# Kernel optimization log

Hardware: AMD Instinct MI355X
Metric: run time of the kernel (lower is better)

Reference implementation:

```python
import jax, jax.numpy as jnp
import numpy as np

B, T, C = 128, 256, 384
H, D = 6, 64

def setup_inputs() -> dict:
    key = jax.random.key(0)
    ks = jax.random.split(key, 6)
    s = 1.0 / np.sqrt(C)
    return {
        "x": jax.random.normal(ks[0], (B, T, C), dtype=jnp.float32),
        "Wq": jax.random.normal(ks[1], (H, C, D), dtype=jnp.float32) * s,
        "Wk": jax.random.normal(ks[2], (H, C, D), dtype=jnp.float32) * s,
        "Wv": jax.random.normal(ks[3], (H, C, D), dtype=jnp.float32) * s,
        "Wp": jax.random.normal(ks[4], (C, C), dtype=jnp.float32) * s,
        "bp": jnp.zeros((C,), dtype=jnp.float32),
    }

def reference(x, Wq, Wk, Wv, Wp, bp):
    # per-head projections (all heads at once): [B,T,C] x [H,C,D] -> [B,H,T,D]
    q = jnp.einsum("btc,hcd->bhtd", x, Wq)
    k = jnp.einsum("btc,hcd->bhtd", x, Wk)
    v = jnp.einsum("btc,hcd->bhtd", x, Wv)
    scale = 1.0 / jnp.sqrt(jnp.asarray(D, dtype=x.dtype))
    # scores [B,H,T,T], causal mask, softmax
    wei = jnp.einsum("bhqd,bhkd->bhqk", q, k) * scale
    causal = jnp.tril(jnp.ones((T, T), dtype=bool))
    wei = jnp.where(causal, wei, -jnp.inf)
    wei = jax.nn.softmax(wei, axis=-1)
    # dropout layers are identity in eval mode
    out = jnp.einsum("bhqk,bhkd->bhqd", wei, v)
    # concat heads: [B,T,H*D]
    out = out.transpose(0, 2, 1, 3).reshape(B, T, H * D)
    return out @ Wp + bp
```

## Files before the change

### kernel.cpp

```cpp
#include <hip/hip_runtime.h>
#include <stdint.h>


typedef __attribute__((ext_vector_type(8))) short bf16x8;
typedef __attribute__((ext_vector_type(4))) float f32x4;
typedef __attribute__((ext_vector_type(16))) float f32x16;

__device__ __forceinline__ unsigned short f2b(float f) {
    union { float f; unsigned int u; } v; v.f = f;
    unsigned int u = v.u + 0x7fffu + ((v.u >> 16) & 1u);
    return (unsigned short)(u >> 16);
}

__device__ __forceinline__ unsigned int pk2(float lo, float hi) {
    return (unsigned int)f2b(lo) | ((unsigned int)f2b(hi) << 16);
}

__device__ __forceinline__ void gload_lds16(const void* g, void* lds) {
    auto gp = reinterpret_cast<const __attribute__((address_space(1))) uint32_t*>(
        reinterpret_cast<uintptr_t>(g));
    auto lp = reinterpret_cast<__attribute__((address_space(3))) uint32_t*>(
        reinterpret_cast<uintptr_t>(lds));
    __builtin_amdgcn_global_load_lds(gp, lp, 16, 0, 0);
}

#define SBAR0() __builtin_amdgcn_sched_barrier(0)


__global__ void cvt_w_kernel(const float* __restrict__ Wq, const float* __restrict__ Wk,
                             const float* __restrict__ Wv, const float* __restrict__ Wp,
                             unsigned short* __restrict__ wt, unsigned short* __restrict__ wpt) {
    int i = blockIdx.x * 256 + threadIdx.x;
    if (i >= 589824) return;
    if (i < 442368) {
        int j = i / 384, c = i - j * 384;
        int p = j / 384, rem = j - p * 384;
        int h = rem >> 6, d = rem & 63;
        const float* W = (p == 0) ? Wq : ((p == 1) ? Wk : Wv);
        wt[i] = f2b(W[(size_t)(h * 384 + c) * 64 + d]);
    } else {
        int i2 = i - 442368;
        int n = i2 / 384, c = i2 - n * 384;
        wpt[i2] = f2b(Wp[(size_t)c * 384 + n]);
    }
}


__global__ __launch_bounds__(256, 4) void gemm_qkv(
    const float* __restrict__ x,
    const unsigned short* __restrict__ wt,
    unsigned short* __restrict__ qO,
    unsigned short* __restrict__ kO,
    unsigned short* __restrict__ vO)
{
    extern __shared__ __align__(16) unsigned short smem[];
    unsigned short* As0 = smem;
    unsigned short* As1 = smem + 4096;
    unsigned short* Bs0 = smem + 8192;
    unsigned short* Bs1 = smem + 12288;

    const int tid  = threadIdx.x;
    const int lane = tid & 63;
    const int w    = tid >> 6;
    const int wm = w >> 1, wn = w & 1;

    const int flat = blockIdx.y * 9 + blockIdx.x;
    const int swz = (flat & 7) * 288 + (flat >> 3);
    const int bx = swz % 9, by = swz / 9;
    const int col0 = bx * 128;
    const int row0 = by * 128;

    f32x4 acc[4][4];
#pragma unroll
    for (int mf = 0; mf < 4; ++mf)
#pragma unroll
        for (int nf = 0; nf < 4; ++nf)
#pragma unroll
            for (int r = 0; r < 4; ++r) acc[mf][nf][r] = 0.f;

    const int ci0 = tid;
    const int ci1 = tid + 256;
    const float* aS0 = x + (size_t)(row0 + (ci0 >> 2)) * 384 + (ci0 & 3) * 8;
    const float* aS1 = x + (size_t)(row0 + (ci1 >> 2)) * 384 + (ci1 & 3) * 8;
    const unsigned short* bS0 = wt + (size_t)(col0 + (ci0 >> 2)) * 384 + (ci0 & 3) * 8;
    const unsigned short* bS1 = wt + (size_t)(col0 + (ci1 >> 2)) * 384 + (ci1 & 3) * 8;
    const int cb = w * 64;

    float4 aReg0, aReg1, aReg2, aReg3;
    auto LOADA = [&](int kt) {
        const float* p0 = aS0 + kt * 32;
        const float* p1 = aS1 + kt * 32;
        aReg0 = *(const float4*)(p0);
        aReg1 = *(const float4*)(p0 + 4);
        aReg2 = *(const float4*)(p1);
        aReg3 = *(const float4*)(p1 + 4);
    };
    auto WRITEA = [&](unsigned short* As) {
        uint4 w0 = make_uint4(pk2(aReg0.x, aReg0.y), pk2(aReg0.z, aReg0.w),
                              pk2(aReg1.x, aReg1.y), pk2(aReg1.z, aReg1.w));
        uint4 w1 = make_uint4(pk2(aReg2.x, aReg2.y), pk2(aReg2.z, aReg2.w),
                              pk2(aReg3.x, aReg3.y), pk2(aReg3.z, aReg3.w));
        *(uint4*)&As[ci0 * 8] = w0;
        *(uint4*)&As[ci1 * 8] = w1;
    };
    auto STAGEB = [&](unsigned short* Bs, int kt) {
        gload_lds16(bS0 + kt * 32, Bs + (cb + 0) * 8);
        gload_lds16(bS1 + kt * 32, Bs + (cb + 256) * 8);
    };
    auto COMPUTE = [&](const unsigned short* A, const unsigned short* B) {
        bf16x8 aF[4], bF[4];
#pragma unroll
        for (int mf = 0; mf < 4; ++mf)
            aF[mf] = *(const bf16x8*)&A[(wm * 64 + mf * 16 + (lane & 15)) * 32 + (lane >> 4) * 8];
#pragma unroll
        for (int nf = 0; nf < 4; ++nf)
            bF[nf] = *(const bf16x8*)&B[(wn * 64 + nf * 16 + (lane & 15)) * 32 + (lane >> 4) * 8];
#pragma unroll
        for (int mf = 0; mf < 4; ++mf)
#pragma unroll
            for (int nf = 0; nf < 4; ++nf)
                acc[mf][nf] = __builtin_amdgcn_mfma_f32_16x16x32_bf16(aF[mf], bF[nf], acc[mf][nf], 0, 0, 0);
    };

    LOADA(0);
    STAGEB(Bs0, 0);
    WRITEA(As0);
    __syncthreads();

    for (int t = 0; t < 12; ++t) {
        unsigned short* Acur = (t & 1) ? As1 : As0;
        unsigned short* Bcur = (t & 1) ? Bs1 : Bs0;
        unsigned short* Anx  = (t & 1) ? As0 : As1;
        unsigned short* Bnx  = (t & 1) ? Bs0 : Bs1;
        if (t < 11) {
            LOADA(t + 1);
            STAGEB(Bnx, t + 1);
        }
        COMPUTE(Acur, Bcur);
        if (t < 11) WRITEA(Anx);
        __syncthreads();
    }

    unsigned short* Ct = smem;
    const int co = tid & 15;
    const int rr = tid >> 4;
    const int colg = col0 + co * 8;
    const int p = colg / 384;
    const int rem = colg - p * 384;
    const int h = rem >> 6;
    const int d = rem & 63;
    unsigned short* dst = (p == 0) ? qO : ((p == 1) ? kO : vO);

#pragma unroll
    for (int ph = 0; ph < 2; ++ph) {
        if (wm == ph) {
#pragma unroll
            for (int mf = 0; mf < 4; ++mf)
#pragma unroll
                for (int nf = 0; nf < 4; ++nf)
#pragma unroll
                    for (int r = 0; r < 4; ++r)
                        Ct[(mf * 16 + (lane >> 4) * 4 + r) * 136 + wn * 64 + nf * 16 + (lane & 15)] =
                            f2b(acc[mf][nf][r]);
        }
        __syncthreads();
#pragma unroll
        for (int it = 0; it < 4; ++it) {
            const int r_loc = it * 16 + rr;
            const int m = row0 + ph * 64 + r_loc;
            const int b = m >> 8, t = m & 255;
            uint4 val = *(const uint4*)&Ct[r_loc * 136 + co * 8];
            *(uint4*)&dst[(size_t)((b * 6 + h) * 256 + t) * 64 + d] = val;
        }
        __syncthreads();
    }
}


__global__ __launch_bounds__(512, 4) void attn_kernel(
    const unsigned short* __restrict__ Qg,
    const unsigned short* __restrict__ Kg,
    const unsigned short* __restrict__ Vg,
    unsigned short* __restrict__ Og)
{
    extern __shared__ __align__(16) unsigned short asmem[];
    unsigned short* Ks = asmem;
    unsigned short* Vs = asmem + 256 * 72;
    unsigned short* Ot = asmem;
    const int bh = blockIdx.x;
    const int b = bh / 6, h = bh - b * 6;
    const int tid = threadIdx.x;
    const int lane = tid & 63;
    const int w = tid >> 6;
    const int lo = lane & 31, hi = lane >> 5;

    const unsigned short* kg = Kg + (size_t)bh * 256 * 64;
#pragma unroll
    for (int j = 0; j < 4; ++j) {
        int chunk = tid + 512 * j;
        int key = chunk >> 3, dc = (chunk & 7) * 8;
        *(uint4*)&Ks[key * 72 + dc] = *(const uint4*)&kg[key * 64 + dc];
    }
    {
        const unsigned short* vg = Vg + (size_t)bh * 256 * 64;
        uint32_t* Vs32 = (uint32_t*)Vs;
#pragma unroll
        for (int i = 0; i < 2; ++i) {
            int u = tid + 512 * i;
            int t2 = (u & 31) | ((u >> 8) << 5);
            int dm = (u >> 5) & 7;
            uint4 r0 = *(const uint4*)&vg[(2 * t2 + 0) * 64 + dm * 8];
            uint4 r1 = *(const uint4*)&vg[(2 * t2 + 1) * 64 + dm * 8];
            const unsigned short* e0 = (const unsigned short*)&r0;
            const unsigned short* e1 = (const unsigned short*)&r1;
#pragma unroll
            for (int j = 0; j < 8; ++j)
                Vs32[(dm * 8 + j) * 132 + t2] = (uint32_t)e0[j] | ((uint32_t)e1[j] << 16);
        }
    }
    __syncthreads();

    const int q0 = w * 32;
    const unsigned short* qg = Qg + (size_t)bh * 256 * 64 + (size_t)(q0 + lo) * 64 + hi * 8;
    bf16x8 qF[4];
#pragma unroll
    for (int dc = 0; dc < 4; ++dc) qF[dc] = *(const bf16x8*)(qg + dc * 16);

    float m = -1e30f, ssum = 0.f;
    f32x16 o0, o1;
#pragma unroll
    for (int r = 0; r < 16; ++r) { o0[r] = 0.f; o1[r] = 0.f; }

    for (int kt = 0; kt <= w; ++kt) {
        f32x16 s;
#pragma unroll
        for (int r = 0; r < 16; ++r) s[r] = 0.f;
#pragma unroll
        for (int dc = 0; dc < 4; ++dc) {
            bf16x8 aK = *(const bf16x8*)&Ks[(kt * 32 + lo) * 72 + dc * 16 + hi * 8];
            s = __builtin_amdgcn_mfma_f32_32x32x16_bf16(aK, qF[dc], s, 0, 0, 0);
        }
        float p[16];
        float pmax = -1e30f;
        const bool diag = (kt == w);
#pragma unroll
        for (int r = 0; r < 16; ++r) {
            float sv = s[r] * 0.125f;
            const int keyl = (r & 3) + 8 * (r >> 2) + 4 * hi;
            if (diag && keyl > lo) sv = -1e30f;
            p[r] = sv;
            pmax = fmaxf(pmax, sv);
        }
        pmax = fmaxf(pmax, __shfl_xor(pmax, 32, 64));
        const float mn = fmaxf(m, pmax);
        const float sf = __expf(m - mn);
        m = mn;
        ssum *= sf;
#pragma unroll
        for (int r = 0; r < 16; ++r) { o0[r] *= sf; o1[r] *= sf; }
        float rs = 0.f;
#pragma unroll
        for (int r = 0; r < 16; ++r) { p[r] = __expf(p[r] - m); rs += p[r]; }
        rs += __shfl_xor(rs, 32, 64);
        ssum += rs;

        union { unsigned short u[16]; bf16x8 v[2]; } P;
        {
            float recv[4];
#pragma unroll
            for (int j2 = 0; j2 < 4; ++j2) {
                float sendv = hi ? p[j2] : p[4 + j2];
                recv[j2] = __shfl_xor(sendv, 32, 64);
            }
#pragma unroll
            for (int i = 0; i < 4; ++i) P.u[i]     = f2b(hi ? recv[i] : p[i]);
#pragma unroll
            for (int i = 0; i < 4; ++i) P.u[4 + i] = f2b(hi ? p[4 + i] : recv[i]);
        }
        {
            float recv[4];
#pragma unroll
            for (int j2 = 0; j2 < 4; ++j2) {
                float sendv = hi ? p[8 + j2] : p[12 + j2];
                recv[j2] = __shfl_xor(sendv, 32, 64);
            }
#pragma unroll
            for (int i = 0; i < 4; ++i) P.u[8 + i]  = f2b(hi ? recv[i] : p[8 + i]);
#pragma unroll
            for (int i = 0; i < 4; ++i) P.u[12 + i] = f2b(hi ? p[12 + i] : recv[i]);
        }

#pragma unroll
        for (int kc = 0; kc < 2; ++kc) {
            bf16x8 aV0 = *(const bf16x8*)&Vs[lo * 264 + kt * 32 + kc * 16 + hi * 8];
            o0 = __builtin_amdgcn_mfma_f32_32x32x16_bf16(aV0, P.v[kc], o0, 0, 0, 0);
            bf16x8 aV1 = *(const bf16x8*)&Vs[(32 + lo) * 264 + kt * 32 + kc * 16 + hi * 8];
            o1 = __builtin_amdgcn_mfma_f32_32x32x16_bf16(aV1, P.v[kc], o1, 0, 0, 0);
        }
    }

    __syncthreads();
    const float inv = 1.f / ssum;
    {
        uint32_t* ot32 = (uint32_t*)&Ot[w * 32 * 72];
#pragma unroll
        for (int g = 0; g < 4; ++g) {
            const int dbase0 = 8 * g + 4 * hi;
            uint32_t w0 = pk2(o0[4 * g + 0] * inv, o0[4 * g + 1] * inv);
            uint32_t w1 = pk2(o0[4 * g + 2] * inv, o0[4 * g + 3] * inv);
            int dw = lo * 36 + (dbase0 >> 1);
            ot32[dw] = w0;
            ot32[dw + 1] = w1;
            uint32_t w2 = pk2(o1[4 * g + 0] * inv, o1[4 * g + 1] * inv);
            uint32_t w3 = pk2(o1[4 * g + 2] * inv, o1[4 * g + 3] * inv);
            int dw1 = lo * 36 + ((32 + dbase0) >> 1);
            ot32[dw1] = w2;
            ot32[dw1 + 1] = w3;
        }
    }
    __syncthreads();
    {
        const unsigned short* ot = &Ot[w * 32 * 72];
        const int q = lane >> 1;
        const int half = (lane & 1) * 32;
        unsigned short* og = Og + (size_t)(b * 256 + q0 + q) * 384 + h * 64 + half;
#pragma unroll
        for (int jj = 0; jj < 4; ++jj) {
            uint4 val = *(const uint4*)&ot[q * 72 + half + jj * 8];
            *(uint4*)&og[jj * 8] = val;
        }
    }
}


__global__ __launch_bounds__(256, 3) void gemm_proj(
    const unsigned short* __restrict__ ob,
    const unsigned short* __restrict__ wpt,
    const float* __restrict__ bp,
    float* __restrict__ out)
{
    __shared__ __align__(16) unsigned short As[3][128 * 32];
    __shared__ __align__(16) unsigned short Bs[3][128 * 32];
    const int tid  = threadIdx.x;
    const int lane = tid & 63;
    const int w    = tid >> 6;
    const int wm = w >> 1, wn = w & 1;

    const int flat = blockIdx.y * 3 + blockIdx.x;
    const int swz = (flat & 7) * 96 + (flat >> 3);
    const int bx = swz % 3, by = swz / 3;
    const int col0 = bx * 128;
    const int row0 = by * 128;

    const unsigned short* Abase = ob  + (size_t)row0 * 384;
    const unsigned short* Bbase = wpt + (size_t)col0 * 384;

    f32x4 acc[4][4];
#pragma unroll
    for (int mf = 0; mf < 4; ++mf)
#pragma unroll
        for (int nf = 0; nf < 4; ++nf)
#pragma unroll
            for (int r = 0; r < 4; ++r) acc[mf][nf][r] = 0.f;

    const int ci0 = tid;
    const int ci1 = tid + 256;
    const unsigned short* aSrc0 = Abase + (size_t)(ci0 >> 2) * 384 + (ci0 & 3) * 8;
    const unsigned short* aSrc1 = Abase + (size_t)(ci1 >> 2) * 384 + (ci1 & 3) * 8;
    const unsigned short* bSrc0 = Bbase + (size_t)(ci0 >> 2) * 384 + (ci0 & 3) * 8;
    const unsigned short* bSrc1 = Bbase + (size_t)(ci1 >> 2) * 384 + (ci1 & 3) * 8;
    const int cb = w * 64;

    auto STAGE = [&](int buf, int kt) {
        const int k0_ = kt * 32;
        gload_lds16(aSrc0 + k0_, (unsigned short*)As[buf] + (cb + 0) * 8);
        gload_lds16(bSrc0 + k0_, (unsigned short*)Bs[buf] + (cb + 0) * 8);
        gload_lds16(aSrc1 + k0_, (unsigned short*)As[buf] + (cb + 256) * 8);
        gload_lds16(bSrc1 + k0_, (unsigned short*)Bs[buf] + (cb + 256) * 8);
    };

    auto COMPUTE = [&](int buf) {
        const unsigned short* A = As[buf];
        const unsigned short* B = Bs[buf];
        bf16x8 aF[4], bF[4];
#pragma unroll
        for (int mf = 0; mf < 4; ++mf)
            aF[mf] = *(const bf16x8*)&A[(wm * 64 + mf * 16 + (lane & 15)) * 32 + (lane >> 4) * 8];
#pragma unroll
        for (int nf = 0; nf < 4; ++nf)
            bF[nf] = *(const bf16x8*)&B[(wn * 64 + nf * 16 + (lane & 15)) * 32 + (lane >> 4) * 8];
#pragma unroll
        for (int mf = 0; mf < 4; ++mf)
#pragma unroll
            for (int nf = 0; nf < 4; ++nf)
                acc[mf][nf] = __builtin_amdgcn_mfma_f32_16x16x32_bf16(aF[mf], bF[nf], acc[mf][nf], 0, 0, 0);
    };

    STAGE(0, 0);
    STAGE(1, 1);
    SBAR0();
    int bufS = 2, bufC = 0;
    for (int t = 0; t < 10; ++t) {
        STAGE(bufS, t + 2);
        bufS = (bufS == 2) ? 0 : bufS + 1;
        SBAR0();
        asm volatile("s_waitcnt vmcnt(8)" ::: "memory");
        SBAR0();
        __builtin_amdgcn_s_barrier();
        SBAR0();
        COMPUTE(bufC);
        bufC = (bufC == 2) ? 0 : bufC + 1;
        SBAR0();
        __builtin_amdgcn_s_barrier();
        SBAR0();
    }
    asm volatile("s_waitcnt vmcnt(4)" ::: "memory");
    SBAR0();
    __builtin_amdgcn_s_barrier();
    SBAR0();
    COMPUTE(1);
    SBAR0();
    __builtin_amdgcn_s_barrier();
    SBAR0();
    asm volatile("s_waitcnt vmcnt(0)" ::: "memory");
    SBAR0();
    __builtin_amdgcn_s_barrier();
    SBAR0();
    COMPUTE(2);

#pragma unroll
    for (int nf = 0; nf < 4; ++nf) {
        const int col = col0 + wn * 64 + nf * 16 + (lane & 15);
        const float bias = bp[col];
#pragma unroll
        for (int mf = 0; mf < 4; ++mf) {
            const int mbase = row0 + wm * 64 + mf * 16 + ((lane >> 4) * 4);
#pragma unroll
            for (int r = 0; r < 4; ++r) {
                const int mrow = mbase + r;
                out[(size_t)mrow * 384 + col] = acc[mf][nf][r] + bias;
            }
        }
    }
}


extern "C" void kernel_launch(void* const* d_in, const int* in_sizes, int n_in,
                              void* d_out, int out_size, void* d_ws, size_t ws_size,
                              hipStream_t stream) {
    const float* x  = (const float*)d_in[0];
    const float* Wq = (const float*)d_in[1];
    const float* Wk = (const float*)d_in[2];
    const float* Wv = (const float*)d_in[3];
    const float* Wp = (const float*)d_in[4];
    const float* bp = (const float*)d_in[5];
    float* out = (float*)d_out;

    char* ws = (char*)d_ws;
    unsigned short* ob  = (unsigned short*)(ws);
    unsigned short* qb  = (unsigned short*)(ws + 25165824);
    unsigned short* kb  = (unsigned short*)(ws + 50331648);
    unsigned short* vb  = (unsigned short*)(ws + 75497472);
    unsigned short* wt  = (unsigned short*)(ws + 100663296);
    unsigned short* wpt = (unsigned short*)(ws + 101548032);

    cvt_w_kernel<<<2304, 256, 0, stream>>>(Wq, Wk, Wv, Wp, wt, wpt);
    gemm_qkv<<<dim3(9, 256), 256, 32768, stream>>>(x, wt, qb, kb, vb);
    attn_kernel<<<768, 512, 70656, stream>>>(qb, kb, vb, ob);
    gemm_proj<<<dim3(3, 256), 256, 0, stream>>>(ob, wpt, bp, out);
}
```

Baseline: 107.8 us.

## Use hardware bf16 pack, MFMA priority, lazy softmax rescale, swizzled LDS in projection

In the QKV GEMM, the manual round-to-nearest bf16 packing is replaced by the v_cvt_pk_bf16_f32 instruction. In the attention loop, MFMA blocks are wrapped in s_setprio, and the online-softmax rescale of the output accumulators now runs only when the running max grows by more than 8. The output projection GEMM XOR-swizzles its global-to-LDS chunk placement and fragment reads to reduce LDS bank conflicts. The lazy rescale keeps a stale max, so exp values can reach up to e^8 before normalisation. That is safe in fp32 but changes the bf16 rounding of P slightly.

Measured after the change: 105.2 us (median of 3 runs). -2.5%, faster.

```diff
diff --git a/kernel.cpp b/kernel.cpp
--- a/kernel.cpp
+++ b/kernel.cpp
@@ -14,6 +14,12 @@
 
 __device__ __forceinline__ unsigned int pk2(float lo, float hi) {
     return (unsigned int)f2b(lo) | ((unsigned int)f2b(hi) << 16);
+}
+
+__device__ __forceinline__ uint32_t cvtpk(float lo, float hi) {
+    uint32_t r;
+    asm("v_cvt_pk_bf16_f32 %0, %1, %2" : "=v"(r) : "v"(lo), "v"(hi));
+    return r;
 }
 
 __device__ __forceinline__ void gload_lds16(const void* g, void* lds) {
@@ -96,10 +102,11 @@
         aReg3 = *(const float4*)(p1 + 4);
     };
     auto WRITEA = [&](unsigned short* As) {
-        uint4 w0 = make_uint4(pk2(aReg0.x, aReg0.y), pk2(aReg0.z, aReg0.w),
-                              pk2(aReg1.x, aReg1.y), pk2(aReg1.z, aReg1.w));
-        uint4 w1 = make_uint4(pk2(aReg2.x, aReg2.y), pk2(aReg2.z, aReg2.w),
-                              pk2(aReg3.x, aReg3.y), pk2(aReg3.z, aReg3.w));
+        uint4 w0, w1;
+        w0.x = cvtpk(aReg0.x, aReg0.y); w0.y = cvtpk(aReg0.z, aReg0.w);
+        w0.z = cvtpk(aReg1.x, aReg1.y); w0.w = cvtpk(aReg1.z, aReg1.w);
+        w1.x = cvtpk(aReg2.x, aReg2.y); w1.y = cvtpk(aReg2.z, aReg2.w);
+        w1.z = cvtpk(aReg3.x, aReg3.y); w1.w = cvtpk(aReg3.z, aReg3.w);
         *(uint4*)&As[ci0 * 8] = w0;
         *(uint4*)&As[ci1 * 8] = w1;
     };
@@ -235,11 +242,13 @@
         f32x16 s;
 #pragma unroll
         for (int r = 0; r < 16; ++r) s[r] = 0.f;
+        __builtin_amdgcn_s_setprio(1);
 #pragma unroll
         for (int dc = 0; dc < 4; ++dc) {
             bf16x8 aK = *(const bf16x8*)&Ks[(kt * 32 + lo) * 72 + dc * 16 + hi * 8];
             s = __builtin_amdgcn_mfma_f32_32x32x16_bf16(aK, qF[dc], s, 0, 0, 0);
         }
+        __builtin_amdgcn_s_setprio(0);
         float p[16];
         float pmax = -1e30f;
         const bool diag = (kt == w);
@@ -252,12 +261,13 @@
             pmax = fmaxf(pmax, sv);
         }
         pmax = fmaxf(pmax, __shfl_xor(pmax, 32, 64));
-        const float mn = fmaxf(m, pmax);
-        const float sf = __expf(m - mn);
-        m = mn;
-        ssum *= sf;
-#pragma unroll
-        for (int r = 0; r < 16; ++r) { o0[r] *= sf; o1[r] *= sf; }
+        if (pmax > m + 8.f) {
+            const float sf = __expf(m - pmax);
+            m = pmax;
+            ssum *= sf;
+#pragma unroll
+            for (int r = 0; r < 16; ++r) { o0[r] *= sf; o1[r] *= sf; }
+        }
         float rs = 0.f;
 #pragma unroll
         for (int r = 0; r < 16; ++r) { p[r] = __expf(p[r] - m); rs += p[r]; }
@@ -290,6 +300,7 @@
             for (int i = 0; i < 4; ++i) P.u[12 + i] = f2b(hi ? p[12 + i] : recv[i]);
         }
 
+        __builtin_amdgcn_s_setprio(1);
 #pragma unroll
         for (int kc = 0; kc < 2; ++kc) {
             bf16x8 aV0 = *(const bf16x8*)&Vs[lo * 264 + kt * 32 + kc * 16 + hi * 8];
@@ -297,6 +308,7 @@
             bf16x8 aV1 = *(const bf16x8*)&Vs[(32 + lo) * 264 + kt * 32 + kc * 16 + hi * 8];
             o1 = __builtin_amdgcn_mfma_f32_32x32x16_bf16(aV1, P.v[kc], o1, 0, 0, 0);
         }
+        __builtin_amdgcn_s_setprio(0);
     }
 
     __syncthreads();
@@ -365,10 +377,12 @@
 
     const int ci0 = tid;
     const int ci1 = tid + 256;
-    const unsigned short* aSrc0 = Abase + (size_t)(ci0 >> 2) * 384 + (ci0 & 3) * 8;
-    const unsigned short* aSrc1 = Abase + (size_t)(ci1 >> 2) * 384 + (ci1 & 3) * 8;
-    const unsigned short* bSrc0 = Bbase + (size_t)(ci0 >> 2) * 384 + (ci0 & 3) * 8;
-    const unsigned short* bSrc1 = Bbase + (size_t)(ci1 >> 2) * 384 + (ci1 & 3) * 8;
+    const int r0c = ci0 >> 2, o0c = (ci0 & 3) ^ ((ci0 >> 3) & 3);
+    const int r1c = ci1 >> 2, o1c = (ci1 & 3) ^ ((ci1 >> 3) & 3);
+    const unsigned short* aSrc0 = Abase + (size_t)r0c * 384 + o0c * 8;
+    const unsigned short* aSrc1 = Abase + (size_t)r1c * 384 + o1c * 8;
+    const unsigned short* bSrc0 = Bbase + (size_t)r0c * 384 + o0c * 8;
+    const unsigned short* bSrc1 = Bbase + (size_t)r1c * 384 + o1c * 8;
     const int cb = w * 64;
 
     auto STAGE = [&](int buf, int kt) {
@@ -379,16 +393,19 @@
         gload_lds16(bSrc1 + k0_, (unsigned short*)Bs[buf] + (cb + 256) * 8);
     };
 
+    const int fr = lane & 15;
+    const int oc = (lane >> 4) ^ ((fr >> 1) & 3);
+
     auto COMPUTE = [&](int buf) {
         const unsigned short* A = As[buf];
         const unsigned short* B = Bs[buf];
         bf16x8 aF[4], bF[4];
 #pragma unroll
         for (int mf = 0; mf < 4; ++mf)
-            aF[mf] = *(const bf16x8*)&A[(wm * 64 + mf * 16 + (lane & 15)) * 32 + (lane >> 4) * 8];
+            aF[mf] = *(const bf16x8*)&A[(wm * 64 + mf * 16 + fr) * 32 + oc * 8];
 #pragma unroll
         for (int nf = 0; nf < 4; ++nf)
-            bF[nf] = *(const bf16x8*)&B[(wn * 64 + nf * 16 + (lane & 15)) * 32 + (lane >> 4) * 8];
+            bF[nf] = *(const bf16x8*)&B[(wn * 64 + nf * 16 + fr) * 32 + oc * 8];
 #pragma unroll
         for (int mf = 0; mf < 4; ++mf)
 #pragma unroll
```
